# Optimization experiments

Hardware: AMD Instinct MI355X
Metric: run time of the kernel (lower is better)

Reference implementation:

```python
import jax, jax.numpy as jnp
import numpy as np

MAX_DIM = 1024
VOCAB = 257
DEPTH = 6
Q_DIM = MAX_DIM // 4  # 256
EXP_DIMS = [1, 2, 4, 8, 16, 32, 64, 128]  # expander sizes: current_q doubles up to Q_DIM
BATCH, SEQ = 8, 4096


def qlinear(q, W):
    """Quaternion Hamilton-product linear.
    q: [..., in, 4] (last dim = r,i,j,k components), W: [4, out, in] (stacked r,i,j,k weights).
    Returns [..., out, 4].
    """
    # P[..., o, w, a] = F.linear(component_a, W_w)  -> all 16 small GEMMs in one einsum
    P = jnp.einsum('...ia,woi->...owa', q, W)
    Pr, Pi, Pj, Pk = P[..., 0, :], P[..., 1, :], P[..., 2, :], P[..., 3, :]  # each [..., out, 4]
    out_r = Pr[..., 0] - Pi[..., 1] - Pj[..., 2] - Pk[..., 3]
    out_i = Pi[..., 0] + Pr[..., 1] + Pk[..., 2] - Pj[..., 3]
    out_j = Pj[..., 0] - Pk[..., 1] + Pr[..., 2] + Pi[..., 3]
    out_k = Pk[..., 0] + Pj[..., 1] - Pi[..., 2] + Pr[..., 3]
    return jnp.stack([out_r, out_i, out_j, out_k], axis=-1)


def qnormalize(q):
    norm = jnp.linalg.norm(q, axis=-1, keepdims=True)
    return q / (norm + 1e-8)


def setup_inputs() -> dict:
    key = jax.random.key(0)
    ks = jax.random.split(key, 4 + len(EXP_DIMS))
    inp = {}
    inp['x'] = jax.random.randint(ks[0], (BATCH, SEQ), 0, VOCAB)
    inp['emb'] = jax.random.normal(ks[1], (VOCAB, 4), dtype=jnp.float32)
    for idx, cq in enumerate(EXP_DIMS):
        scale = cq ** (-0.5)
        inp[f'w_exp{idx}'] = jax.random.uniform(ks[2 + idx], (4, cq, cq), jnp.float32, -scale, scale)
    scale = Q_DIM ** (-0.5)
    inp['w_layers'] = jax.random.uniform(ks[-2], (DEPTH, 4, Q_DIM, Q_DIM), jnp.float32, -scale, scale)
    inp['w_head'] = jax.random.normal(ks[-1], (VOCAB, MAX_DIM), dtype=jnp.float32) * MAX_DIM ** (-0.5)
    return inp


def reference(x, emb, w_exp0, w_exp1, w_exp2, w_exp3, w_exp4, w_exp5, w_exp6, w_exp7,
              w_layers, w_head):
    q = emb[x][:, :, None, :]  # [B, S, 1, 4]
    for w in (w_exp0, w_exp1, w_exp2, w_exp3, w_exp4, w_exp5, w_exp6, w_exp7):
        delta = jnp.tanh(qlinear(q, w))
        q = jnp.concatenate([q + delta, q - delta], axis=2)  # doubles quaternion dim
    for d in range(DEPTH):
        q = qnormalize(qlinear(q, w_layers[d]))
    stability_loss = jnp.mean(jnp.abs(q[..., 0]))
    h_flat = q.reshape(x.shape[0], x.shape[1], -1)  # [B, S, MAX_DIM]
    logits = jnp.einsum('bsd,vd->bsv', h_flat, w_head)
    return (logits, stability_loss)
```

## Files before the change

### kernel.cpp

```cpp
#include <hip/hip_runtime.h>


typedef _Float16 f16x8 __attribute__((ext_vector_type(8)));
typedef float    f32x4 __attribute__((ext_vector_type(4)));

#define GL2LDS16(gp, lp) __builtin_amdgcn_global_load_lds(                     \
    (const __attribute__((address_space(1))) void*)(gp),                       \
    (__attribute__((address_space(3))) void*)(lp), 16, 0, 0)

__device__ __forceinline__ unsigned short f2h(float f) {
  union { _Float16 h; unsigned short u; } c;
  c.h = (_Float16)f;
  return c.u;
}
__device__ __forceinline__ float h2f(unsigned short u) {
  union { unsigned short u; _Float16 h; } c;
  c.u = u;
  return (float)c.h;
}

__global__ __launch_bounds__(256) void expand_ham(
    const float* __restrict__ w, unsigned short* __restrict__ out,
    int cq, int kbits, int total) {
  int id = blockIdx.x * 256 + threadIdx.x;
  if (id >= total) return;
  const int K = 1 << kbits;
  const int n = id >> kbits;
  const int k = id & (K - 1);
  float val = 0.f;
  if (n < 4 * cq) {
    const int o = n >> 2, a = n & 3, i = k >> 2, b = k & 3;
    const int   comp[4][4] = {{0,1,2,3},{1,0,3,2},{2,3,0,1},{3,2,1,0}};
    const float sgn [4][4] = {{1.f,-1.f,-1.f,-1.f},{1.f,1.f,1.f,-1.f},
                              {1.f,-1.f,1.f,1.f},{1.f,1.f,-1.f,1.f}};
    val = sgn[a][b] * w[comp[a][b] * cq * cq + o * cq + i];
  }
  out[id] = f2h(val);
}

__global__ __launch_bounds__(256) void conv_head(
    const float* __restrict__ wh, unsigned short* __restrict__ out) {
  int id = blockIdx.x * 256 + threadIdx.x;
  int v = id >> 10, k = id & 1023;
  out[id] = f2h(v < 257 ? wh[v * 1024 + k] : 0.f);
}

template <int CQ>
__device__ __forceinline__ void exp_step(float (&q)[16][4],
                                         const float* __restrict__ w) {
  float d[CQ][4];
#pragma unroll
  for (int o = 0; o < CQ; o++) {
    float pr = 0.f, pi = 0.f, pj = 0.f, pk = 0.f;
#pragma unroll
    for (int i = 0; i < CQ; i++) {
      const float wr = w[0 * CQ * CQ + o * CQ + i];
      const float wi = w[1 * CQ * CQ + o * CQ + i];
      const float wj = w[2 * CQ * CQ + o * CQ + i];
      const float wk = w[3 * CQ * CQ + o * CQ + i];
      const float qr = q[i][0], qi = q[i][1], qj = q[i][2], qk = q[i][3];
      pr += wr * qr - wi * qi - wj * qj - wk * qk;
      pi += wi * qr + wr * qi + wk * qj - wj * qk;
      pj += wj * qr - wk * qi + wr * qj + wi * qk;
      pk += wk * qr + wj * qi - wi * qj + wr * qk;
    }
    d[o][0] = tanhf(pr); d[o][1] = tanhf(pi);
    d[o][2] = tanhf(pj); d[o][3] = tanhf(pk);
  }
#pragma unroll
  for (int o = 0; o < CQ; o++)
#pragma unroll
    for (int a = 0; a < 4; a++) {
      const float dd = d[o][a], qq = q[o][a];
      q[o][a]      = qq + dd;
      q[CQ + o][a] = qq - dd;
    }
}

__global__ __launch_bounds__(256) void embed_expand(
    const int* __restrict__ x, const float* __restrict__ emb,
    const float* __restrict__ w0, const float* __restrict__ w1,
    const float* __restrict__ w2, const float* __restrict__ w3,
    unsigned short* __restrict__ out) {
  const int t = blockIdx.x * 256 + threadIdx.x;
  float q[16][4];
  const int v = x[t];
  const float4 e = *(const float4*)(emb + v * 4);
  q[0][0] = e.x; q[0][1] = e.y; q[0][2] = e.z; q[0][3] = e.w;
  exp_step<1>(q, w0);
  exp_step<2>(q, w1);
  exp_step<4>(q, w2);
  exp_step<8>(q, w3);
  ushort4* o4 = (ushort4*)(out + (size_t)t * 64);
#pragma unroll
  for (int c = 0; c < 16; c++) {
    ushort4 u;
    u.x = f2h(q[c][0]); u.y = f2h(q[c][1]);
    u.z = f2h(q[c][2]); u.w = f2h(q[c][3]);
    o4[c] = u;
  }
}

template <int EPI>
__global__ __launch_bounds__(256) void gemm_epi(
    const unsigned short* __restrict__ W,
    const unsigned short* __restrict__ Act,
    unsigned short* __restrict__ OutB, float* __restrict__ OutF,
    int K, int Nreal, int ldout) {
  __shared__ unsigned short WtL[128 * 32];
  __shared__ unsigned short WtH[128 * 32];
  __shared__ unsigned short AtL[128 * 32];
  __shared__ unsigned short AtH[128 * 32];
  __shared__ float lsum[4];

  const int tid  = threadIdx.x;
  const int wave = tid >> 6;
  const int lane = tid & 63;
  const int l15  = lane & 15;
  const int quad = lane >> 4;

  const int Gx = gridDim.x;
  const int L  = blockIdx.y * Gx + blockIdx.x;
  const int j  = L & 7;
  const int s  = L >> 3;
  const int nblock = (s % Gx) * 128;
  const int mblock = (32 * j + s / Gx) * 128;
  const int wn = (wave & 1) * 64;
  const int wm = (wave >> 1) * 64;

  f32x4 acc[4][4];
  const f32x4 zero = {0.f, 0.f, 0.f, 0.f};
#pragma unroll
  for (int a = 0; a < 4; a++)
#pragma unroll
    for (int b = 0; b < 4; b++) acc[a][b] = zero;

  const int row0 = tid >> 2;
  const int sub  = tid & 3;
  const unsigned short* gW0 = W   + (size_t)(nblock + row0)      * K + sub * 8;
  const unsigned short* gW1 = W   + (size_t)(nblock + row0 + 64) * K + sub * 8;
  const unsigned short* gA0 = Act + (size_t)(mblock + row0)      * K + sub * 8;
  const unsigned short* gA1 = Act + (size_t)(mblock + row0 + 64) * K + sub * 8;
  unsigned short* lWL0 = &WtL[wave * 512];
  unsigned short* lWL1 = &WtL[2048 + wave * 512];
  unsigned short* lWH0 = &WtH[wave * 512];
  unsigned short* lWH1 = &WtH[2048 + wave * 512];
  unsigned short* lAL0 = &AtL[wave * 512];
  unsigned short* lAL1 = &AtL[2048 + wave * 512];
  unsigned short* lAH0 = &AtH[wave * 512];
  unsigned short* lAH1 = &AtH[2048 + wave * 512];

  for (int kb = 0; kb < K; kb += 64) {
    GL2LDS16(gW0 + kb,      lWL0);
    GL2LDS16(gW1 + kb,      lWL1);
    GL2LDS16(gW0 + kb + 32, lWH0);
    GL2LDS16(gW1 + kb + 32, lWH1);
    GL2LDS16(gA0 + kb,      lAL0);
    GL2LDS16(gA1 + kb,      lAL1);
    GL2LDS16(gA0 + kb + 32, lAH0);
    GL2LDS16(gA1 + kb + 32, lAH1);
    __syncthreads();

    {
      f16x8 afr[4], bfr[4];
#pragma unroll
      for (int tn = 0; tn < 4; tn++)
        afr[tn] = *(const f16x8*)&WtL[(wn + tn * 16 + l15) * 32 + quad * 8];
#pragma unroll
      for (int tm = 0; tm < 4; tm++)
        bfr[tm] = *(const f16x8*)&AtL[(wm + tm * 16 + l15) * 32 + quad * 8];
#pragma unroll
      for (int tn = 0; tn < 4; tn++)
#pragma unroll
        for (int tm = 0; tm < 4; tm++)
          acc[tn][tm] = __builtin_amdgcn_mfma_f32_16x16x32_f16(
              afr[tn], bfr[tm], acc[tn][tm], 0, 0, 0);
    }
    {
      f16x8 afr[4], bfr[4];
#pragma unroll
      for (int tn = 0; tn < 4; tn++)
        afr[tn] = *(const f16x8*)&WtH[(wn + tn * 16 + l15) * 32 + quad * 8];
#pragma unroll
      for (int tm = 0; tm < 4; tm++)
        bfr[tm] = *(const f16x8*)&AtH[(wm + tm * 16 + l15) * 32 + quad * 8];
#pragma unroll
      for (int tn = 0; tn < 4; tn++)
#pragma unroll
        for (int tm = 0; tm < 4; tm++)
          acc[tn][tm] = __builtin_amdgcn_mfma_f32_16x16x32_f16(
              afr[tn], bfr[tm], acc[tn][tm], 0, 0, 0);
    }
    __syncthreads();
  }

  if constexpr (EPI == 0) {
#pragma unroll
    for (int tn = 0; tn < 4; tn++) {
      const int n = nblock + wn + tn * 16 + quad * 4;
      if (n < Nreal) {
#pragma unroll
        for (int tm = 0; tm < 4; tm++) {
          const int token = mblock + wm + tm * 16 + l15;
          const f32x4 v = acc[tn][tm];
          const unsigned short* ip = Act + (size_t)token * K + n;
          const float i0 = h2f(ip[0]), i1 = h2f(ip[1]);
          const float i2 = h2f(ip[2]), i3 = h2f(ip[3]);
          const float d0 = tanhf(v[0]), d1 = tanhf(v[1]);
          const float d2 = tanhf(v[2]), d3 = tanhf(v[3]);
          ushort4 up, um;
          up.x = f2h(i0 + d0); up.y = f2h(i1 + d1);
          up.z = f2h(i2 + d2); up.w = f2h(i3 + d3);
          um.x = f2h(i0 - d0); um.y = f2h(i1 - d1);
          um.z = f2h(i2 - d2); um.w = f2h(i3 - d3);
          *(ushort4*)&OutB[(size_t)token * ldout + n] = up;
          *(ushort4*)&OutB[(size_t)token * ldout + Nreal + n] = um;
        }
      }
    }
  } else if constexpr (EPI == 1 || EPI == 2) {
    float loss = 0.f;
#pragma unroll
    for (int tn = 0; tn < 4; tn++) {
      const int n = nblock + wn + tn * 16 + quad * 4;
#pragma unroll
      for (int tm = 0; tm < 4; tm++) {
        const int token = mblock + wm + tm * 16 + l15;
        const f32x4 v = acc[tn][tm];
        const float nrm =
            sqrtf(v[0] * v[0] + v[1] * v[1] + v[2] * v[2] + v[3] * v[3]);
        const float inv = 1.f / (nrm + 1e-8f);
        ushort4 u;
        u.x = f2h(v[0] * inv); u.y = f2h(v[1] * inv);
        u.z = f2h(v[2] * inv); u.w = f2h(v[3] * inv);
        *(ushort4*)&OutB[(size_t)token * ldout + n] = u;
        if constexpr (EPI == 2) loss += fabsf(v[0] * inv);
      }
    }
    if constexpr (EPI == 2) {
#pragma unroll
      for (int off = 32; off > 0; off >>= 1) loss += __shfl_down(loss, off);
      if (lane == 0) lsum[wave] = loss;
      __syncthreads();
      if (tid == 0)
        atomicAdd(OutF,
                  (lsum[0] + lsum[1] + lsum[2] + lsum[3]) * (1.f / 8388608.f));
    }
  } else {
#pragma unroll
    for (int tn = 0; tn < 4; tn++) {
      const int n = nblock + wn + tn * 16 + quad * 4;
      if (n < 257) {
#pragma unroll
        for (int tm = 0; tm < 4; tm++) {
          const int token = mblock + wm + tm * 16 + l15;
          const f32x4 v = acc[tn][tm];
#pragma unroll
          for (int r = 0; r < 4; r++)
            if (n + r < 257) OutF[(size_t)token * 257 + n + r] = v[r];
        }
      }
    }
  }
}

extern "C" void kernel_launch(void* const* d_in, const int* in_sizes, int n_in,
                              void* d_out, int out_size, void* d_ws,
                              size_t ws_size, hipStream_t stream) {
  const int*   x    = (const int*)d_in[0];
  const float* emb  = (const float*)d_in[1];
  const float* we0  = (const float*)d_in[2];
  const float* we1  = (const float*)d_in[3];
  const float* we2  = (const float*)d_in[4];
  const float* we3  = (const float*)d_in[5];
  const float* we4  = (const float*)d_in[6];
  const float* we5  = (const float*)d_in[7];
  const float* we6  = (const float*)d_in[8];
  const float* we7  = (const float*)d_in[9];
  const float* wlay = (const float*)d_in[10];
  const float* wh   = (const float*)d_in[11];
  float* out = (float*)d_out;

  char* p = (char*)d_ws;
  auto alloc = [&](size_t bytes) {
    void* r = (void*)p;
    p += (bytes + 255) & ~(size_t)255;
    return r;
  };
  unsigned short* act0 = (unsigned short*)alloc(32768ull * 1024 * 2);
  unsigned short* act1 = (unsigned short*)alloc(32768ull * 1024 * 2);
  unsigned short* E4 = (unsigned short*)alloc(128 * 64 * 2);
  unsigned short* E5 = (unsigned short*)alloc(128 * 128 * 2);
  unsigned short* E6 = (unsigned short*)alloc(256 * 256 * 2);
  unsigned short* E7 = (unsigned short*)alloc(512 * 512 * 2);
  unsigned short* EL = (unsigned short*)alloc(6ull * 1024 * 1024 * 2);
  unsigned short* WH = (unsigned short*)alloc(384 * 1024 * 2);

  hipMemsetAsync(out + 8421376, 0, 4, stream);

  expand_ham<<<dim3(8192 / 256), 256, 0, stream>>>(we4, E4, 16, 6, 128 * 64);
  expand_ham<<<dim3(16384 / 256), 256, 0, stream>>>(we5, E5, 32, 7, 128 * 128);
  expand_ham<<<dim3(65536 / 256), 256, 0, stream>>>(we6, E6, 64, 8, 256 * 256);
  expand_ham<<<dim3(262144 / 256), 256, 0, stream>>>(we7, E7, 128, 9,
                                                     512 * 512);
  for (int d = 0; d < 6; d++)
    expand_ham<<<dim3(1048576 / 256), 256, 0, stream>>>(
        wlay + (size_t)d * 262144, EL + (size_t)d * 1048576, 256, 10, 1048576);
  conv_head<<<dim3(384 * 1024 / 256), 256, 0, stream>>>(wh, WH);

  embed_expand<<<dim3(128), 256, 0, stream>>>(x, emb, we0, we1, we2, we3, act0);

  gemm_epi<0><<<dim3(1, 256), 256, 0, stream>>>(E4, act0, act1, nullptr, 64,
                                                64, 128);
  gemm_epi<0><<<dim3(1, 256), 256, 0, stream>>>(E5, act1, act0, nullptr, 128,
                                                128, 256);
  gemm_epi<0><<<dim3(2, 256), 256, 0, stream>>>(E6, act0, act1, nullptr, 256,
                                                256, 512);
  gemm_epi<0><<<dim3(4, 256), 256, 0, stream>>>(E7, act1, act0, nullptr, 512,
                                                512, 1024);

  unsigned short* a = act0;
  unsigned short* b = act1;
  for (int d = 0; d < 5; d++) {
    gemm_epi<1><<<dim3(8, 256), 256, 0, stream>>>(EL + (size_t)d * 1048576, a,
                                                  b, nullptr, 1024, 1024, 1024);
    unsigned short* t = a; a = b; b = t;
  }
  gemm_epi<2><<<dim3(8, 256), 256, 0, stream>>>(EL + 5ull * 1048576, a, b,
                                                out + 8421376, 1024, 1024,
                                                1024);
  { unsigned short* t = a; a = b; b = t; }

  gemm_epi<3><<<dim3(3, 256), 256, 0, stream>>>(WH, a, nullptr, out, 1024, 257,
                                                0);
}
```

Measured before the change: 856.7 us.

## Add 256x256-tile 8-wave GEMM with 4-stage LDS pipeline for layer and head GEMMs

Introduces a new gemm8p kernel using 512 threads, 256x256 output tiles, a four-stage global-to-LDS prefetch ring with explicit vmcnt waits, swizzled LDS reads, and setprio around MFMA bursts. The depth layers and the logits head now use it instead of the 128x128 gemm_epi, which is reduced to the expander epilogue only. The aim is more operand reuse per LDS load and better overlap of memory with MFMA. In exchange it uses 128KB of LDS per block and large accumulator register pressure, and the head pads N to 384 with clamped weight rows.

```diff
diff --git a/kernel.cpp b/kernel.cpp
--- a/kernel.cpp
+++ b/kernel.cpp
@@ -111,7 +111,6 @@
   __shared__ unsigned short WtH[128 * 32];
   __shared__ unsigned short AtL[128 * 32];
   __shared__ unsigned short AtH[128 * 32];
-  __shared__ float lsum[4];
 
   const int tid  = threadIdx.x;
   const int wave = tid >> 6;
@@ -194,38 +193,151 @@
     __syncthreads();
   }
 
-  if constexpr (EPI == 0) {
-#pragma unroll
-    for (int tn = 0; tn < 4; tn++) {
-      const int n = nblock + wn + tn * 16 + quad * 4;
-      if (n < Nreal) {
-#pragma unroll
-        for (int tm = 0; tm < 4; tm++) {
-          const int token = mblock + wm + tm * 16 + l15;
-          const f32x4 v = acc[tn][tm];
-          const unsigned short* ip = Act + (size_t)token * K + n;
-          const float i0 = h2f(ip[0]), i1 = h2f(ip[1]);
-          const float i2 = h2f(ip[2]), i3 = h2f(ip[3]);
-          const float d0 = tanhf(v[0]), d1 = tanhf(v[1]);
-          const float d2 = tanhf(v[2]), d3 = tanhf(v[3]);
-          ushort4 up, um;
-          up.x = f2h(i0 + d0); up.y = f2h(i1 + d1);
-          up.z = f2h(i2 + d2); up.w = f2h(i3 + d3);
-          um.x = f2h(i0 - d0); um.y = f2h(i1 - d1);
-          um.z = f2h(i2 - d2); um.w = f2h(i3 - d3);
-          *(ushort4*)&OutB[(size_t)token * ldout + n] = up;
-          *(ushort4*)&OutB[(size_t)token * ldout + Nreal + n] = um;
-        }
-      }
-    }
-  } else if constexpr (EPI == 1 || EPI == 2) {
-    float loss = 0.f;
-#pragma unroll
-    for (int tn = 0; tn < 4; tn++) {
-      const int n = nblock + wn + tn * 16 + quad * 4;
+#pragma unroll
+  for (int tn = 0; tn < 4; tn++) {
+    const int n = nblock + wn + tn * 16 + quad * 4;
+    if (n < Nreal) {
 #pragma unroll
       for (int tm = 0; tm < 4; tm++) {
         const int token = mblock + wm + tm * 16 + l15;
+        const f32x4 v = acc[tn][tm];
+        const unsigned short* ip = Act + (size_t)token * K + n;
+        const float i0 = h2f(ip[0]), i1 = h2f(ip[1]);
+        const float i2 = h2f(ip[2]), i3 = h2f(ip[3]);
+        const float d0 = tanhf(v[0]), d1 = tanhf(v[1]);
+        const float d2 = tanhf(v[2]), d3 = tanhf(v[3]);
+        ushort4 up, um;
+        up.x = f2h(i0 + d0); up.y = f2h(i1 + d1);
+        up.z = f2h(i2 + d2); up.w = f2h(i3 + d3);
+        um.x = f2h(i0 - d0); um.y = f2h(i1 - d1);
+        um.z = f2h(i2 - d2); um.w = f2h(i3 - d3);
+        *(ushort4*)&OutB[(size_t)token * ldout + n] = up;
+        *(ushort4*)&OutB[(size_t)token * ldout + Nreal + n] = um;
+      }
+    }
+  }
+}
+
+template <int EPI>
+__global__ __launch_bounds__(512, 2) void gemm8p(
+    const unsigned short* __restrict__ W,
+    const unsigned short* __restrict__ Act,
+    unsigned short* __restrict__ OutB, float* __restrict__ OutF,
+    int K, int NW) {
+  __shared__ unsigned short S[65536];
+  __shared__ float lsum[8];
+
+  const int tid  = threadIdx.x;
+  const int wave = tid >> 6;
+  const int lane = tid & 63;
+  const int l15  = lane & 15;
+  const int quad = lane >> 4;
+  const int wr   = wave >> 2;
+  const int wc   = wave & 3;
+
+  const int Gx = gridDim.x;
+  const int L  = blockIdx.y * Gx + blockIdx.x;
+  const int j  = L & 7;
+  const int s  = L >> 3;
+  const int mtile = j * (gridDim.y >> 3) + s / Gx;
+  const int ntile = s % Gx;
+  const int nblock = ntile * 256;
+  const int mblock = mtile * 256;
+
+  const int NT = K >> 5;
+
+  f32x4 acc[8][4];
+  const f32x4 zero = {0.f, 0.f, 0.f, 0.f};
+#pragma unroll
+  for (int a = 0; a < 8; a++)
+#pragma unroll
+    for (int b = 0; b < 4; b++) acc[a][b] = zero;
+
+  const int rA = tid >> 2;
+  const int sl = (tid & 3) ^ ((tid >> 3) & 3);
+  const int w0r = nblock + rA;
+  const int w1r = nblock + 128 + rA;
+  const int cw0 = w0r < NW ? w0r : NW - 1;
+  const int cw1 = w1r < NW ? w1r : NW - 1;
+  const unsigned short* sW0 = W   + (size_t)cw0 * K + sl * 8;
+  const unsigned short* sW1 = W   + (size_t)cw1 * K + sl * 8;
+  const unsigned short* sA0 = Act + (size_t)(mblock + rA)       * K + sl * 8;
+  const unsigned short* sA1 = Act + (size_t)(mblock + 128 + rA) * K + sl * 8;
+
+  const int swz = (quad * 8) ^ ((l15 & 6) << 2);
+
+  for (int t = 0; t < 3 && t < NT; ++t) {
+    const int kb = t * 32;
+    unsigned short* d = S + t * 16384 + tid * 8;
+    GL2LDS16(sW0 + kb, d);
+    GL2LDS16(sA0 + kb, d + 8192);
+    GL2LDS16(sW1 + kb, d + 4096);
+    GL2LDS16(sA1 + kb, d + 12288);
+  }
+  if (NT >= 3)      asm volatile("s_waitcnt vmcnt(8)" ::: "memory");
+  else if (NT == 2) asm volatile("s_waitcnt vmcnt(4)" ::: "memory");
+  else              asm volatile("s_waitcnt vmcnt(0)" ::: "memory");
+  __builtin_amdgcn_s_barrier();
+
+  for (int kt = 0; kt < NT; ++kt) {
+    const unsigned short* SA = S + (kt & 3) * 16384;
+    const unsigned short* SB = SA + 8192;
+    const int  nxt = (kt + 3) & 3;
+    const bool pf  = (kt + 3) < NT;
+    const int  kb  = (kt + 3) * 32;
+    unsigned short* d = S + nxt * 16384 + tid * 8;
+
+    f16x8 af[4], bf[4];
+#pragma unroll
+    for (int t4 = 0; t4 < 4; t4++)
+      af[t4] = *(const f16x8*)(SA + (wr * 128 + t4 * 16 + l15) * 32 + swz);
+#pragma unroll
+    for (int t4 = 0; t4 < 4; t4++)
+      bf[t4] = *(const f16x8*)(SB + (wc * 64 + t4 * 16 + l15) * 32 + swz);
+    if (pf) { GL2LDS16(sW0 + kb, d); GL2LDS16(sA0 + kb, d + 8192); }
+    __builtin_amdgcn_s_barrier();
+    asm volatile("s_waitcnt lgkmcnt(0)" ::: "memory");
+    __builtin_amdgcn_sched_barrier(0);
+    __builtin_amdgcn_s_setprio(1);
+#pragma unroll
+    for (int tn = 0; tn < 4; tn++)
+#pragma unroll
+      for (int tm = 0; tm < 4; tm++)
+        acc[tn][tm] = __builtin_amdgcn_mfma_f32_16x16x32_f16(
+            af[tn], bf[tm], acc[tn][tm], 0, 0, 0);
+    __builtin_amdgcn_s_setprio(0);
+    __builtin_amdgcn_s_barrier();
+#pragma unroll
+    for (int t4 = 0; t4 < 4; t4++)
+      af[t4] = *(const f16x8*)(SA + (wr * 128 + 64 + t4 * 16 + l15) * 32 + swz);
+    if (pf) { GL2LDS16(sW1 + kb, d + 4096); GL2LDS16(sA1 + kb, d + 12288); }
+    __builtin_amdgcn_s_barrier();
+    asm volatile("s_waitcnt lgkmcnt(0)" ::: "memory");
+    __builtin_amdgcn_sched_barrier(0);
+    __builtin_amdgcn_s_setprio(1);
+#pragma unroll
+    for (int tn = 0; tn < 4; tn++)
+#pragma unroll
+      for (int tm = 0; tm < 4; tm++)
+        acc[4 + tn][tm] = __builtin_amdgcn_mfma_f32_16x16x32_f16(
+            af[tn], bf[tm], acc[4 + tn][tm], 0, 0, 0);
+    __builtin_amdgcn_s_setprio(0);
+    if (kt < NT - 1) {
+      if (kt + 3 < NT)       asm volatile("s_waitcnt vmcnt(8)" ::: "memory");
+      else if (kt + 3 == NT) asm volatile("s_waitcnt vmcnt(4)" ::: "memory");
+      else                   asm volatile("s_waitcnt vmcnt(0)" ::: "memory");
+      __builtin_amdgcn_s_barrier();
+    }
+  }
+
+  if constexpr (EPI == 1 || EPI == 2) {
+    float loss = 0.f;
+#pragma unroll
+    for (int tn = 0; tn < 8; tn++) {
+      const int n = nblock + wr * 128 + tn * 16 + quad * 4;
+#pragma unroll
+      for (int tm = 0; tm < 4; tm++) {
+        const int token = mblock + wc * 64 + tm * 16 + l15;
         const f32x4 v = acc[tn][tm];
         const float nrm =
             sqrtf(v[0] * v[0] + v[1] * v[1] + v[2] * v[2] + v[3] * v[3]);
@@ -233,7 +345,7 @@
         ushort4 u;
         u.x = f2h(v[0] * inv); u.y = f2h(v[1] * inv);
         u.z = f2h(v[2] * inv); u.w = f2h(v[3] * inv);
-        *(ushort4*)&OutB[(size_t)token * ldout + n] = u;
+        *(ushort4*)&OutB[(size_t)token * 1024 + n] = u;
         if constexpr (EPI == 2) loss += fabsf(v[0] * inv);
       }
     }
@@ -242,18 +354,21 @@
       for (int off = 32; off > 0; off >>= 1) loss += __shfl_down(loss, off);
       if (lane == 0) lsum[wave] = loss;
       __syncthreads();
-      if (tid == 0)
-        atomicAdd(OutF,
-                  (lsum[0] + lsum[1] + lsum[2] + lsum[3]) * (1.f / 8388608.f));
+      if (tid == 0) {
+        float t = 0.f;
+#pragma unroll
+        for (int w8 = 0; w8 < 8; w8++) t += lsum[w8];
+        atomicAdd(OutF, t * (1.f / 8388608.f));
+      }
     }
   } else {
 #pragma unroll
-    for (int tn = 0; tn < 4; tn++) {
-      const int n = nblock + wn + tn * 16 + quad * 4;
+    for (int tn = 0; tn < 8; tn++) {
+      const int n = nblock + wr * 128 + tn * 16 + quad * 4;
       if (n < 257) {
 #pragma unroll
         for (int tm = 0; tm < 4; tm++) {
-          const int token = mblock + wm + tm * 16 + l15;
+          const int token = mblock + wc * 64 + tm * 16 + l15;
           const f32x4 v = acc[tn][tm];
 #pragma unroll
           for (int r = 0; r < 4; r++)
@@ -322,15 +437,13 @@
   unsigned short* a = act0;
   unsigned short* b = act1;
   for (int d = 0; d < 5; d++) {
-    gemm_epi<1><<<dim3(8, 256), 256, 0, stream>>>(EL + (size_t)d * 1048576, a,
-                                                  b, nullptr, 1024, 1024, 1024);
+    gemm8p<1><<<dim3(4, 128), 512, 0, stream>>>(EL + (size_t)d * 1048576, a, b,
+                                                nullptr, 1024, 1024);
     unsigned short* t = a; a = b; b = t;
   }
-  gemm_epi<2><<<dim3(8, 256), 256, 0, stream>>>(EL + 5ull * 1048576, a, b,
-                                                out + 8421376, 1024, 1024,
-                                                1024);
+  gemm8p<2><<<dim3(4, 128), 512, 0, stream>>>(EL + 5ull * 1048576, a, b,
+                                              out + 8421376, 1024, 1024);
   { unsigned short* t = a; a = b; b = t; }
 
-  gemm_epi<3><<<dim3(3, 256), 256, 0, stream>>>(WH, a, nullptr, out, 1024, 257,
-                                                0);
-}
+  gemm8p<3><<<dim3(2, 128), 512, 0, stream>>>(WH, a, nullptr, out, 1024, 384);
+}
```

Measured after the change: 819.8 us. 4.3% less time.
